# Optimization experiments

Hardware: AMD Instinct MI355X
Metric: run time of the kernel (lower is better)

The kernel has to match this reference:

```python
import jax, jax.numpy as jnp
import numpy as np

SIG = [1, 1, 1, 1, -1]  # Cl(4,1)
NVEC = 5
GA = 1 << NVEC  # 32


def _build_gp_table():
    # Cayley table for the geometric product on blades indexed by bitmask.
    G = np.zeros((GA, GA, GA), np.float32)
    for a in range(GA):
        for b in range(GA):
            s = 0
            t = a >> 1
            while t:
                s += bin(t & b).count('1')
                t >>= 1
            sign = -1.0 if (s & 1) else 1.0
            common = a & b
            for i in range(NVEC):
                if (common >> i) & 1:
                    sign *= SIG[i]
            G[a, b, a ^ b] = sign
    return G

GP_TABLE = jnp.asarray(_build_gp_table())


def geometric_product(x, y):
    return jnp.einsum('...i,...j,ijk->...k', x, y, GP_TABLE)


def manifold_norm(x):
    # normalize each multivector onto the unit sphere in R^32
    return x / (jnp.linalg.norm(x, axis=-1, keepdims=True) + 1e-6)


def versor_linear(x, W, b):
    # channel mixing shared across multivector components: x [..., in, ga]
    return jnp.einsum('...ig,oi->...og', x, W) + b


def layer_norm2d(x, w, b):
    # LayerNorm over last two dims [D, ga] jointly
    mu = jnp.mean(x, axis=(-2, -1), keepdims=True)
    var = jnp.var(x, axis=(-2, -1), keepdims=True)
    return (x - mu) / jnp.sqrt(var + 1e-5) * w + b


def attention(x, Wq, bq, Wk, bk, Wv, bv, Wo, bo, n_heads):
    B, S, D, G = x.shape
    dh = D // n_heads
    q = versor_linear(x, Wq, bq).reshape(B, S, n_heads, dh, G)
    k = versor_linear(x, Wk, bk).reshape(B, S, n_heads, dh, G)
    v = versor_linear(x, Wv, bv).reshape(B, S, n_heads, dh, G)
    scale = 1.0 / np.sqrt(dh * G).astype(np.float32)
    scores = jnp.einsum('bshdg,bthdg->bhst', q, k) * scale
    probs = jax.nn.softmax(scores, axis=-1)
    o = jnp.einsum('bhst,bthdg->bshdg', probs, v).reshape(B, S, D, G)
    return versor_linear(o, Wo, bo)


N_HEADS = 8


def forward(x, Wq, bq, Wk, bk, Wv, bv, Wo, bo, ln1_w, ln1_b, ln2_w, ln2_b,
            gamma1, gamma2, W1, b1, W2, b2, Wr, br, Wc, bc):
    L = Wq.shape[0]
    for l in range(L):
        h = attention(layer_norm2d(x, ln1_w[l], ln1_b[l]),
                      Wq[l], bq[l], Wk[l], bk[l], Wv[l], bv[l], Wo[l], bo[l], N_HEADS)
        x = manifold_norm(x + gamma1[l] * h)
        m = versor_linear(layer_norm2d(x, ln2_w[l], ln2_b[l]), W1[l], b1[l])
        m = versor_linear(jnp.tanh(m), W2[l], b2[l])
        x = manifold_norm(x + gamma2[l] * m)
    # RecursiveRotorAccumulator: log(S)-step inclusive scan of rotors
    delta = versor_linear(x, Wr, br)
    rot = 0.5 * delta
    rot = rot.at[..., 0].add(1.0)
    rot = manifold_norm(rot)
    S = x.shape[1]
    step = 1
    while step < S:
        left = rot[:, :-step]
        right = rot[:, step:]
        comb = manifold_norm(geometric_product(right, left))
        rot = jnp.concatenate([rot[:, :step], comb], axis=1)
        step *= 2
    pooled = rot[:, -1]  # [B, D, ga]
    logits = pooled.reshape(pooled.shape[0], -1) @ Wc.T + bc
    return logits


def setup_inputs() -> dict:
    key = jax.random.key(0)
    B, S, D, G, L, NC = 8, 256, 64, GA, 4, 1000
    E = 4 * D  # expansion hidden
    ks = jax.random.split(key, 16)
    sd = 0.02
    inp = {
        'x': jax.random.normal(ks[0], (B, S, D, G), jnp.float32),
        'Wq': jax.random.normal(ks[1], (L, D, D), jnp.float32) * sd,
        'bq': jnp.zeros((L, D, G), jnp.float32),
        'Wk': jax.random.normal(ks[2], (L, D, D), jnp.float32) * sd,
        'bk': jnp.zeros((L, D, G), jnp.float32),
        'Wv': jax.random.normal(ks[3], (L, D, D), jnp.float32) * sd,
        'bv': jnp.zeros((L, D, G), jnp.float32),
        'Wo': jax.random.normal(ks[4], (L, D, D), jnp.float32) * sd,
        'bo': jnp.zeros((L, D, G), jnp.float32),
        'ln1_w': jnp.ones((L, D, G), jnp.float32),
        'ln1_b': jnp.zeros((L, D, G), jnp.float32),
        'ln2_w': jnp.ones((L, D, G), jnp.float32),
        'ln2_b': jnp.zeros((L, D, G), jnp.float32),
        'gamma1': 1e-5 * jnp.ones((L, D, G), jnp.float32),
        'gamma2': 1e-5 * jnp.ones((L, D, G), jnp.float32),
        'W1': jax.random.normal(ks[5], (L, E, D), jnp.float32) * sd,
        'b1': jnp.zeros((L, E, G), jnp.float32),
        'W2': jax.random.normal(ks[6], (L, D, E), jnp.float32) * sd,
        'b2': jnp.zeros((L, D, G), jnp.float32),
        'Wr': jax.random.normal(ks[7], (D, D), jnp.float32) * sd,
        'br': jnp.zeros((D, G), jnp.float32),
        'Wc': jax.random.normal(ks[8], (NC, D * G), jnp.float32) * sd,
        'bc': jnp.zeros((NC,), jnp.float32),
    }
    return inp


def reference(x, Wq, bq, Wk, bk, Wv, bv, Wo, bo, ln1_w, ln1_b, ln2_w, ln2_b,
              gamma1, gamma2, W1, b1, W2, b2, Wr, br, Wc, bc):
    return forward(x, Wq, bq, Wk, bk, Wv, bv, Wo, bo, ln1_w, ln1_b, ln2_w, ln2_b,
                   gamma1, gamma2, W1, b1, W2, b2, Wr, br, Wc, bc)
```

## Files before the change

### kernel.cpp

```cpp
#include <hip/hip_runtime.h>
#include <hip/hip_bf16.h>

constexpr int kB  = 8;
constexpr int kS  = 256;
constexpr int kD  = 64;
constexpr int kG  = 32;
constexpr int kE  = 256;
constexpr int kNH = 8;
constexpr int kHD = 256;
constexpr int kDG = kD * kG;
constexpr int kT  = kB * kS;
constexpr int kNC = 1000;

using bf16x8 = __attribute__((ext_vector_type(8))) short;
using f32x4  = __attribute__((ext_vector_type(4))) float;

__device__ __forceinline__ short f2bf(float f) {
    unsigned u = __float_as_uint(f);
    unsigned r = (u + 0x7FFFu + ((u >> 16) & 1u)) >> 16;
    return (short)r;
}

__device__ __forceinline__ float tanh_fast(float x) {
    float a = fabsf(x);
    float e = __expf(-2.f * a);
    float t = (1.f - e) / (1.f + e);
    return copysignf(t, x);
}

__global__ __launch_bounds__(256) void cvtw_kernel(
    const float* __restrict__ Wq, const float* __restrict__ Wk,
    const float* __restrict__ Wv, const float* __restrict__ Wo,
    const float* __restrict__ W1, const float* __restrict__ W2,
    unsigned short* __restrict__ dst) {
    int idx = (blockIdx.x * 256 + threadIdx.x) * 4;
    const float* src; int off;
    if      (idx <  16384) { src = Wq; off = 0; }
    else if (idx <  32768) { src = Wk; off = 16384; }
    else if (idx <  49152) { src = Wv; off = 32768; }
    else if (idx <  65536) { src = Wo; off = 49152; }
    else if (idx < 131072) { src = W1; off = 65536; }
    else                   { src = W2; off = 131072; }
    const float4 v = *(const float4*)(src + (idx - off));
    *(short4*)&dst[idx] = make_short4(f2bf(v.x), f2bf(v.y), f2bf(v.z), f2bf(v.w));
}

__global__ __launch_bounds__(256) void ln_kernel(const float* __restrict__ Xin,
                                                 const float* __restrict__ w,
                                                 const float* __restrict__ b,
                                                 float* __restrict__ A) {
    int t = blockIdx.x, tid = threadIdx.x;
    const float* xp = Xin + (size_t)t * kDG;
    __shared__ float r1[256], r2[256];
    float v[8], s = 0.f, ss = 0.f;
#pragma unroll
    for (int j = 0; j < 8; j++) {
        float x = xp[tid + j * 256];
        v[j] = x; s += x; ss += x * x;
    }
    r1[tid] = s; r2[tid] = ss; __syncthreads();
    for (int o = 128; o > 0; o >>= 1) {
        if (tid < o) { r1[tid] += r1[tid + o]; r2[tid] += r2[tid + o]; }
        __syncthreads();
    }
    float mean = r1[0] * (1.f / kDG);
    float var  = r2[0] * (1.f / kDG) - mean * mean;
    float rstd = rsqrtf(var + 1e-5f);
    float* ao = A + (size_t)t * kDG;
#pragma unroll
    for (int j = 0; j < 8; j++) {
        int jj = tid + j * 256;
        ao[jj] = (v[j] - mean) * rstd * w[jj] + b[jj];
    }
}

__device__ __forceinline__ void epi_res_mn_ln(
    const f32x4 (&acc)[4][2], const float* __restrict__ bias,
    const float* __restrict__ Xin, float* __restrict__ Xout,
    const float* __restrict__ gamma,
    const float* __restrict__ lnw, const float* __restrict__ lnb,
    float* __restrict__ Aout, int tok, int l16, int quad, bool do_ln) {
    const size_t tb = (size_t)tok * kDG;
    float xv[4][2][4];
    float s = 0.f, ss = 0.f;
#pragma unroll
    for (int mt = 0; mt < 4; ++mt)
#pragma unroll
        for (int r = 0; r < 4; ++r) {
            int o = mt * 16 + quad * 4 + r;
            float vv[2]; float sq = 0.f;
#pragma unroll
            for (int nt = 0; nt < 2; ++nt) {
                int g = nt * 16 + l16;
                float h = acc[mt][nt][r] + bias[o * kG + g];
                float v = Xin[tb + o * kG + g] + gamma[o * kG + g] * h;
                vv[nt] = v; sq = fmaf(v, v, sq);
            }
#pragma unroll
            for (int off = 1; off < 16; off <<= 1) sq += __shfl_xor(sq, off, 64);
            float rn = 1.f / (sqrtf(sq) + 1e-6f);
#pragma unroll
            for (int nt = 0; nt < 2; ++nt) {
                int g = nt * 16 + l16;
                float x = vv[nt] * rn;
                xv[mt][nt][r] = x;
                Xout[tb + o * kG + g] = x;
                s += x; ss = fmaf(x, x, ss);
            }
        }
    if (!do_ln) return;
#pragma unroll
    for (int off = 1; off < 64; off <<= 1) {
        s += __shfl_xor(s, off, 64); ss += __shfl_xor(ss, off, 64);
    }
    float mean = s * (1.f / kDG);
    float var  = ss * (1.f / kDG) - mean * mean;
    float rstd = rsqrtf(var + 1e-5f);
#pragma unroll
    for (int mt = 0; mt < 4; ++mt)
#pragma unroll
        for (int nt = 0; nt < 2; ++nt) {
            int g = nt * 16 + l16;
#pragma unroll
            for (int r = 0; r < 4; ++r) {
                int o = mt * 16 + quad * 4 + r;
                Aout[tb + o * kG + g] = (xv[mt][nt][r] - mean) * rstd * lnw[o * kG + g] + lnb[o * kG + g];
            }
        }
}

__global__ __launch_bounds__(256) void vlinT_kernel(const float* __restrict__ X,
                                                    const float* __restrict__ W,
                                                    const float* __restrict__ bias,
                                                    float* __restrict__ OutT) {
    __shared__ float sx[kDG];
    __shared__ float sw[kD * kD];
    int t = blockIdx.x, tid = threadIdx.x;
    const float* xp = X + (size_t)t * kDG;
    for (int j = tid; j < kDG; j += 256) sx[j] = xp[j];
    for (int j = tid; j < kD * kD; j += 256) sw[j] = W[j];
    __syncthreads();
    int g = tid & 31, ob = tid >> 5;
    int b = t >> 8, s = t & 255;
    float* op = OutT + ((size_t)b * kD * kS + s) * kG;
    for (int o = ob; o < kD; o += 8) {
        float acc = bias[o * kG + g];
        const float* wr = sw + o * kD;
#pragma unroll
        for (int i = 0; i < kD; i++) acc += wr[i] * sx[i * kG + g];
        op[(size_t)o * kS * kG + g] = acc;
    }
}

__global__ __launch_bounds__(256, 2) void mlp1_kernel(
    const float* __restrict__ X, const unsigned short* __restrict__ Wh,
    const float* __restrict__ bias, unsigned short* __restrict__ outH) {
    constexpr int M = 256;
    constexpr int WS = 64 + 8;
    __shared__ short sW[M * WS];
    __shared__ short sXT[4][32][WS];

    const int tid = threadIdx.x, wave = tid >> 6, lane = tid & 63;
    const int l16 = lane & 15, quad = lane >> 4;
    const int tok = blockIdx.x * 4 + wave;

    for (int j = tid * 8; j < M * 64; j += 2048) {
        int o = j >> 6, i = j & 63;
        *(bf16x8*)&sW[o * WS + i] = *(const bf16x8*)(Wh + j);
    }
    {
        const int g4 = (lane & 7) * 4;
        const int i0 = (lane >> 3) * 8;
        const float* xp = X + (size_t)tok * kDG;
#pragma unroll
        for (int half = 0; half < 2; ++half) {
            float4 vr[4];
#pragma unroll
            for (int r = 0; r < 4; ++r)
                vr[r] = *(const float4*)(xp + (i0 + half * 4 + r) * kG + g4);
#pragma unroll
            for (int gg = 0; gg < 4; ++gg)
                *(short4*)&sXT[wave][g4 + gg][i0 + half * 4] =
                    make_short4(f2bf((&vr[0].x)[gg]), f2bf((&vr[1].x)[gg]),
                                f2bf((&vr[2].x)[gg]), f2bf((&vr[3].x)[gg]));
        }
    }
    __syncthreads();

    bf16x8 bfr[2][2];
#pragma unroll
    for (int c = 0; c < 2; ++c)
#pragma unroll
        for (int nt = 0; nt < 2; ++nt)
            bfr[c][nt] = *(const bf16x8*)&sXT[wave][nt * 16 + l16][c * 32 + quad * 8];

    f32x4 acc[16][2];
#pragma unroll
    for (int mt = 0; mt < 16; ++mt)
#pragma unroll
        for (int nt = 0; nt < 2; ++nt) acc[mt][nt] = (f32x4){0.f, 0.f, 0.f, 0.f};

#pragma unroll
    for (int mt = 0; mt < 16; ++mt)
#pragma unroll
        for (int c = 0; c < 2; ++c) {
            bf16x8 afr = *(const bf16x8*)&sW[(mt * 16 + l16) * WS + c * 32 + quad * 8];
#pragma unroll
            for (int nt = 0; nt < 2; ++nt)
                acc[mt][nt] = __builtin_amdgcn_mfma_f32_16x16x32_bf16(afr, bfr[c][nt], acc[mt][nt], 0, 0, 0);
        }

    unsigned short* op = outH + (size_t)tok * M * kG;
#pragma unroll
    for (int mt = 0; mt < 16; ++mt)
#pragma unroll
        for (int nt = 0; nt < 2; ++nt) {
            int g = nt * 16 + l16;
            int e0 = mt * 16 + quad * 4;
            short4 s4;
            s4.x = f2bf(tanh_fast(acc[mt][nt][0] + bias[(e0 + 0) * kG + g]));
            s4.y = f2bf(tanh_fast(acc[mt][nt][1] + bias[(e0 + 1) * kG + g]));
            s4.z = f2bf(tanh_fast(acc[mt][nt][2] + bias[(e0 + 2) * kG + g]));
            s4.w = f2bf(tanh_fast(acc[mt][nt][3] + bias[(e0 + 3) * kG + g]));
            *(short4*)&op[g * M + e0] = s4;
        }
}

__global__ __launch_bounds__(256, 2) void gemmWo_fused_kernel(
    const float* __restrict__ X, const unsigned short* __restrict__ Wh,
    const float* __restrict__ bias,
    const float* __restrict__ Xin, const float* __restrict__ gamma,
    const float* __restrict__ lnw, const float* __restrict__ lnb,
    float* __restrict__ Xout, float* __restrict__ Aout) {
    constexpr int WS = 64 + 8;
    __shared__ short sW[64 * WS];
    __shared__ short sXT[4][32][WS];

    const int tid = threadIdx.x, wave = tid >> 6, lane = tid & 63;
    const int l16 = lane & 15, quad = lane >> 4;
    const int tok = blockIdx.x * 4 + wave;

    for (int j = tid * 8; j < 64 * 64; j += 2048) {
        int o = j >> 6, i = j & 63;
        *(bf16x8*)&sW[o * WS + i] = *(const bf16x8*)(Wh + j);
    }
    {
        const int g4 = (lane & 7) * 4;
        const int i0 = (lane >> 3) * 8;
        const float* xp = X + (size_t)tok * kDG;
#pragma unroll
        for (int half = 0; half < 2; ++half) {
            float4 vr[4];
#pragma unroll
            for (int r = 0; r < 4; ++r)
                vr[r] = *(const float4*)(xp + (i0 + half * 4 + r) * kG + g4);
#pragma unroll
            for (int gg = 0; gg < 4; ++gg)
                *(short4*)&sXT[wave][g4 + gg][i0 + half * 4] =
                    make_short4(f2bf((&vr[0].x)[gg]), f2bf((&vr[1].x)[gg]),
                                f2bf((&vr[2].x)[gg]), f2bf((&vr[3].x)[gg]));
        }
    }
    __syncthreads();

    bf16x8 bfr[2][2];
#pragma unroll
    for (int c = 0; c < 2; ++c)
#pragma unroll
        for (int nt = 0; nt < 2; ++nt)
            bfr[c][nt] = *(const bf16x8*)&sXT[wave][nt * 16 + l16][c * 32 + quad * 8];

    f32x4 acc[4][2];
#pragma unroll
    for (int mt = 0; mt < 4; ++mt)
#pragma unroll
        for (int nt = 0; nt < 2; ++nt) acc[mt][nt] = (f32x4){0.f, 0.f, 0.f, 0.f};

#pragma unroll
    for (int mt = 0; mt < 4; ++mt)
#pragma unroll
        for (int c = 0; c < 2; ++c) {
            bf16x8 afr = *(const bf16x8*)&sW[(mt * 16 + l16) * WS + c * 32 + quad * 8];
#pragma unroll
            for (int nt = 0; nt < 2; ++nt)
                acc[mt][nt] = __builtin_amdgcn_mfma_f32_16x16x32_bf16(afr, bfr[c][nt], acc[mt][nt], 0, 0, 0);
        }

    epi_res_mn_ln(acc, bias, Xin, Xout, gamma, lnw, lnb, Aout, tok, l16, quad, true);
}

__global__ __launch_bounds__(256, 2) void gemm_qkv_kernel(
    const float* __restrict__ X,
    const unsigned short* __restrict__ Wqh, const unsigned short* __restrict__ Wkh,
    const unsigned short* __restrict__ Wvh,
    const float* __restrict__ bq, const float* __restrict__ bk, const float* __restrict__ bv,
    unsigned short* __restrict__ Q, unsigned short* __restrict__ K, unsigned short* __restrict__ V) {
    constexpr int WS = 64 + 8;
    __shared__ short sW[3 * 64 * WS];
    __shared__ short sXT[4][32][WS];

    const int tid = threadIdx.x, wave = tid >> 6, lane = tid & 63;
    const int l16 = lane & 15, quad = lane >> 4;
    const int tok = blockIdx.x * 4 + wave;

    const unsigned short* Wp[3] = {Wqh, Wkh, Wvh};
#pragma unroll
    for (int w = 0; w < 3; ++w)
        for (int j = tid * 8; j < 64 * 64; j += 2048) {
            int o = j >> 6, i = j & 63;
            *(bf16x8*)&sW[w * 64 * WS + o * WS + i] = *(const bf16x8*)(Wp[w] + j);
        }
    {
        const int g4 = (lane & 7) * 4;
        const int i0 = (lane >> 3) * 8;
        const float* xp = X + (size_t)tok * kDG;
#pragma unroll
        for (int half = 0; half < 2; ++half) {
            float4 vr[4];
#pragma unroll
            for (int r = 0; r < 4; ++r)
                vr[r] = *(const float4*)(xp + (i0 + half * 4 + r) * kG + g4);
#pragma unroll
            for (int gg = 0; gg < 4; ++gg)
                *(short4*)&sXT[wave][g4 + gg][i0 + half * 4] =
                    make_short4(f2bf((&vr[0].x)[gg]), f2bf((&vr[1].x)[gg]),
                                f2bf((&vr[2].x)[gg]), f2bf((&vr[3].x)[gg]));
        }
    }
    __syncthreads();

    bf16x8 bfr[2][2];
#pragma unroll
    for (int c = 0; c < 2; ++c)
#pragma unroll
        for (int nt = 0; nt < 2; ++nt)
            bfr[c][nt] = *(const bf16x8*)&sXT[wave][nt * 16 + l16][c * 32 + quad * 8];

    f32x4 acc[3][4][2];
#pragma unroll
    for (int w = 0; w < 3; ++w)
#pragma unroll
        for (int mt = 0; mt < 4; ++mt)
#pragma unroll
            for (int nt = 0; nt < 2; ++nt) acc[w][mt][nt] = (f32x4){0.f, 0.f, 0.f, 0.f};

#pragma unroll
    for (int w = 0; w < 3; ++w)
#pragma unroll
        for (int mt = 0; mt < 4; ++mt)
#pragma unroll
            for (int c = 0; c < 2; ++c) {
                bf16x8 afr = *(const bf16x8*)&sW[w * 64 * WS + (mt * 16 + l16) * WS + c * 32 + quad * 8];
#pragma unroll
                for (int nt = 0; nt < 2; ++nt)
                    acc[w][mt][nt] = __builtin_amdgcn_mfma_f32_16x16x32_bf16(afr, bfr[c][nt], acc[w][mt][nt], 0, 0, 0);
            }

    unsigned short* Op[3] = {Q, K, V};
    const float* Bp[3] = {bq, bk, bv};
#pragma unroll
    for (int w = 0; w < 3; ++w) {
        unsigned short* op = Op[w] + (size_t)tok * kDG;
#pragma unroll
        for (int mt = 0; mt < 4; ++mt)
#pragma unroll
            for (int nt = 0; nt < 2; ++nt) {
                int g = nt * 16 + l16;
#pragma unroll
                for (int r = 0; r < 4; ++r) {
                    int o = mt * 16 + quad * 4 + r;
                    op[o * kG + g] = (unsigned short)f2bf(acc[w][mt][nt][r] + Bp[w][o * kG + g]);
                }
            }
    }
}

template<bool DO_LN>
__global__ __launch_bounds__(256, 2) void mlp2_fused_kernel(
    const unsigned short* __restrict__ Mb,
    const unsigned short* __restrict__ W2h, const float* __restrict__ b2,
    float* __restrict__ X, const float* __restrict__ gamma,
    const float* __restrict__ lnw, const float* __restrict__ lnb,
    float* __restrict__ Aout) {
    constexpr int WS = 256 + 8;
    __shared__ short sW[64 * WS];
    const int tid = threadIdx.x, wave = tid >> 6, lane = tid & 63;
    const int l16 = lane & 15, quad = lane >> 4;
    const int tok = blockIdx.x * 4 + wave;

    for (int j = tid * 8; j < 64 * 256; j += 2048) {
        int o = j >> 8, i = j & 255;
        *(bf16x8*)&sW[o * WS + i] = *(const bf16x8*)(W2h + j);
    }
    __syncthreads();

    f32x4 acc[4][2];
#pragma unroll
    for (int mt = 0; mt < 4; ++mt)
#pragma unroll
        for (int nt = 0; nt < 2; ++nt) acc[mt][nt] = (f32x4){0.f, 0.f, 0.f, 0.f};

    const unsigned short* mp = Mb + (size_t)tok * kG * kE;
#pragma unroll
    for (int c = 0; c < 8; ++c) {
        bf16x8 bfr[2];
#pragma unroll
        for (int nt = 0; nt < 2; ++nt)
            bfr[nt] = *(const bf16x8*)&mp[(nt * 16 + l16) * kE + c * 32 + quad * 8];
#pragma unroll
        for (int mt = 0; mt < 4; ++mt) {
            bf16x8 afr = *(const bf16x8*)&sW[(mt * 16 + l16) * WS + c * 32 + quad * 8];
#pragma unroll
            for (int nt = 0; nt < 2; ++nt)
                acc[mt][nt] = __builtin_amdgcn_mfma_f32_16x16x32_bf16(afr, bfr[nt], acc[mt][nt], 0, 0, 0);
        }
    }

    epi_res_mn_ln(acc, b2, X, X, gamma, lnw, lnb, Aout, tok, l16, quad, DO_LN);
}

constexpr int QSTR = 264;
constexpr int VSTR = 40;

__global__ __launch_bounds__(256) void attn_mfma_kernel(const unsigned short* __restrict__ Q,
                                                        const unsigned short* __restrict__ K,
                                                        const unsigned short* __restrict__ V,
                                                        float* __restrict__ O) {
    __shared__ short sQ[64 * QSTR];
    __shared__ short sKV[256 * VSTR];

    const int qt = blockIdx.x, h = blockIdx.y, b = blockIdx.z;
    const int tid = threadIdx.x;
    const int wave = tid >> 6, lane = tid & 63;
    const int l16 = lane & 15, quad = lane >> 4;

    const size_t bh = (size_t)b * kS * kDG + (size_t)h * kHD;

#pragma unroll
    for (int it = 0; it < 8; ++it) {
        int j = it * 2048 + tid * 8;
        int row = j >> 8, col = j & 255;
        *(bf16x8*)&sQ[row * QSTR + col] =
            *(const bf16x8*)(Q + bh + (size_t)(qt * 64 + row) * kDG + col);
    }
    bf16x8 kpre[4];
#pragma unroll
    for (int it = 0; it < 4; ++it) {
        int j = it * 2048 + tid * 8;
        int row = j >> 8, col = j & 255;
        kpre[it] = *(const bf16x8*)(K + bh + (size_t)row * kDG + col);
    }
    __syncthreads();

    bf16x8 afrag[8];
    {
        int row = wave * 16 + l16;
#pragma unroll
        for (int c = 0; c < 8; ++c)
            afrag[c] = *(const bf16x8*)&sQ[row * QSTR + c * 32 + quad * 8];
    }

    f32x4 acc[16];
#pragma unroll
    for (int i = 0; i < 16; ++i) acc[i] = (f32x4){0.f, 0.f, 0.f, 0.f};

    for (int kt = 0; kt < 8; ++kt) {
#pragma unroll
        for (int it = 0; it < 4; ++it) {
            int j = it * 2048 + tid * 8;
            int row = j >> 8, col = j & 255;
            *(bf16x8*)&sKV[row * QSTR + col] = kpre[it];
        }
        __syncthreads();
        if (kt < 7) {
#pragma unroll
            for (int it = 0; it < 4; ++it) {
                int j = it * 2048 + tid * 8;
                int row = j >> 8, col = j & 255;
                kpre[it] = *(const bf16x8*)(K + bh + (size_t)((kt + 1) * 32 + row) * kDG + col);
            }
        }
#pragma unroll
        for (int nt = 0; nt < 2; ++nt) {
            int key = nt * 16 + l16;
            f32x4 a = acc[kt * 2 + nt];
#pragma unroll
            for (int c = 0; c < 8; ++c) {
                bf16x8 bfrag = *(const bf16x8*)&sKV[key * QSTR + c * 32 + quad * 8];
                a = __builtin_amdgcn_mfma_f32_16x16x32_bf16(afrag[c], bfrag, a, 0, 0, 0);
            }
            acc[kt * 2 + nt] = a;
        }
        __syncthreads();
    }

    float inv[4];
#pragma unroll
    for (int r = 0; r < 4; ++r) {
        float m = -1e30f;
#pragma unroll
        for (int t = 0; t < 16; ++t) m = fmaxf(m, acc[t][r]);
#pragma unroll
        for (int off = 1; off < 16; off <<= 1) m = fmaxf(m, __shfl_xor(m, off, 16));
        float s = 0.f;
#pragma unroll
        for (int t = 0; t < 16; ++t) {
            float p = __expf((acc[t][r] - m) * 0.0625f);
            acc[t][r] = p; s += p;
        }
#pragma unroll
        for (int off = 1; off < 16; off <<= 1) s += __shfl_xor(s, off, 16);
        inv[r] = 1.f / s;
    }

#pragma unroll
    for (int t = 0; t < 16; ++t)
#pragma unroll
        for (int r = 0; r < 4; ++r)
            sQ[(wave * 16 + quad * 4 + r) * QSTR + t * 16 + l16] = f2bf(acc[t][r]);

    short4 vpre[8];
    {
        int kb = tid >> 5;
#pragma unroll
        for (int it = 0; it < 2; ++it) {
            int db = (tid & 31) + it * 32;
#pragma unroll
            for (int r = 0; r < 4; ++r)
                vpre[it * 4 + r] = *(const short4*)(V + bh + (size_t)(kb * 4 + r) * kDG + db * 4);
        }
    }

    f32x4 oacc[16];
#pragma unroll
    for (int i = 0; i < 16; ++i) oacc[i] = (f32x4){0.f, 0.f, 0.f, 0.f};

    for (int vt = 0; vt < 8; ++vt) {
        __syncthreads();
        {
            int kb = tid >> 5;
#pragma unroll
            for (int it = 0; it < 2; ++it) {
                int db = (tid & 31) + it * 32;
#pragma unroll
                for (int i = 0; i < 4; ++i) {
                    short4 p = make_short4((&vpre[it * 4 + 0].x)[i], (&vpre[it * 4 + 1].x)[i],
                                           (&vpre[it * 4 + 2].x)[i], (&vpre[it * 4 + 3].x)[i]);
                    *(short4*)&sKV[(db * 4 + i) * VSTR + kb * 4] = p;
                }
            }
        }
        __syncthreads();
        if (vt < 7) {
            int kb = tid >> 5;
#pragma unroll
            for (int it = 0; it < 2; ++it) {
                int db = (tid & 31) + it * 32;
#pragma unroll
                for (int r = 0; r < 4; ++r)
                    vpre[it * 4 + r] = *(const short4*)(V + bh + (size_t)((vt + 1) * 32 + kb * 4 + r) * kDG + db * 4);
            }
        }
        bf16x8 pfrag = *(const bf16x8*)&sQ[(wave * 16 + l16) * QSTR + vt * 32 + quad * 8];
#pragma unroll
        for (int dt = 0; dt < 16; ++dt) {
            bf16x8 vfrag = *(const bf16x8*)&sKV[(dt * 16 + l16) * VSTR + quad * 8];
            oacc[dt] = __builtin_amdgcn_mfma_f32_16x16x32_bf16(pfrag, vfrag, oacc[dt], 0, 0, 0);
        }
    }

    {
        int qrow = qt * 64 + wave * 16 + quad * 4;
#pragma unroll
        for (int dt = 0; dt < 16; ++dt)
#pragma unroll
            for (int r = 0; r < 4; ++r)
                O[bh + (size_t)(qrow + r) * kDG + dt * 16 + l16] = oacc[dt][r] * inv[r];
    }
}

constexpr int pc_ce(unsigned v) { int c = 0; while (v) { c += v & 1; v >>= 1; } return c; }
constexpr unsigned gp_mask_ce(int a) {
    unsigned m = 0;
    for (int c = 0; c < 32; ++c) {
        int b = a ^ c;
        int s = (a & b) >> 4;
        for (int t = a >> 1; t; t >>= 1) s += pc_ce(t & b);
        if (s & 1) m |= (1u << c);
    }
    return m;
}

template<int A>
__device__ __forceinline__ void gp_term(const float* x, const float* y, float* acc) {
    constexpr unsigned m = gp_mask_ce(A);
    const float xa = x[A], nxa = -xa;
#pragma unroll
    for (int c = 0; c < 32; ++c)
        acc[c] = fmaf(((m >> c) & 1u) ? nxa : xa, y[A ^ c], acc[c]);
}

__device__ __forceinline__ void gp_mn_t(const float* x, const float* y, float* out) {
    float acc[32];
#pragma unroll
    for (int c = 0; c < 32; ++c) acc[c] = 0.f;
    gp_term<0>(x, y, acc);  gp_term<1>(x, y, acc);  gp_term<2>(x, y, acc);  gp_term<3>(x, y, acc);
    gp_term<4>(x, y, acc);  gp_term<5>(x, y, acc);  gp_term<6>(x, y, acc);  gp_term<7>(x, y, acc);
    gp_term<8>(x, y, acc);  gp_term<9>(x, y, acc);  gp_term<10>(x, y, acc); gp_term<11>(x, y, acc);
    gp_term<12>(x, y, acc); gp_term<13>(x, y, acc); gp_term<14>(x, y, acc); gp_term<15>(x, y, acc);
    gp_term<16>(x, y, acc); gp_term<17>(x, y, acc); gp_term<18>(x, y, acc); gp_term<19>(x, y, acc);
    gp_term<20>(x, y, acc); gp_term<21>(x, y, acc); gp_term<22>(x, y, acc); gp_term<23>(x, y, acc);
    gp_term<24>(x, y, acc); gp_term<25>(x, y, acc); gp_term<26>(x, y, acc); gp_term<27>(x, y, acc);
    gp_term<28>(x, y, acc); gp_term<29>(x, y, acc); gp_term<30>(x, y, acc); gp_term<31>(x, y, acc);
    float ss = 0.f;
#pragma unroll
    for (int c = 0; c < 32; ++c) ss = fmaf(acc[c], acc[c], ss);
    float r = 1.f / (sqrtf(ss) + 1e-6f);
#pragma unroll
    for (int c = 0; c < 32; ++c) out[c] = acc[c] * r;
}

__device__ __forceinline__ void leaf_load(const float* base, float* v) {
#pragma unroll
    for (int i = 0; i < 8; ++i) {
        const float4 f = *(const float4*)(base + i * 4);
        v[i * 4 + 0] = 0.5f * f.x; v[i * 4 + 1] = 0.5f * f.y;
        v[i * 4 + 2] = 0.5f * f.z; v[i * 4 + 3] = 0.5f * f.w;
    }
    v[0] += 1.f;
    float ss = 0.f;
#pragma unroll
    for (int c = 0; c < 32; ++c) ss = fmaf(v[c], v[c], ss);
    float r = 1.f / (sqrtf(ss) + 1e-6f);
#pragma unroll
    for (int c = 0; c < 32; ++c) v[c] *= r;
}

__global__ __launch_bounds__(256) void scanreg_kernel(const float* __restrict__ DT,
                                                      float* __restrict__ pooled) {
    const int wave = threadIdx.x >> 6, lane = threadIdx.x & 63;
    const int seq = blockIdx.x * 4 + wave;
    const float* base = DT + ((size_t)seq * kS + lane * 4) * kG;

    float R[32], Y[32], P[32], Xa[32], Yb[32];

    leaf_load(base, R);
    for (int j = 1; j < 4; ++j) {
        leaf_load(base + j * kG, Y);
        gp_mn_t(Y, R, R);
    }

    for (int step = 1; step < 64; step <<= 1) {
        const bool up = lane & step;
#pragma unroll
        for (int c = 0; c < 32; ++c) P[c] = __shfl_xor(R[c], step, 64);
#pragma unroll
        for (int c = 0; c < 32; ++c) {
            Xa[c] = up ? R[c] : P[c];
            Yb[c] = up ? P[c] : R[c];
        }
        gp_mn_t(Xa, Yb, R);
    }

    if (lane == 0) {
        float* op = pooled + (size_t)seq * kG;
#pragma unroll
        for (int i = 0; i < 8; ++i)
            *(float4*)(op + i * 4) = make_float4(R[i * 4], R[i * 4 + 1], R[i * 4 + 2], R[i * 4 + 3]);
    }
}

__global__ __launch_bounds__(256) void cls2_kernel(const float* __restrict__ P,
                                                   const float* __restrict__ Wc,
                                                   const float* __restrict__ bc,
                                                   float* __restrict__ out) {
    __shared__ float sp[kB * kDG];
    const int tid = threadIdx.x, wave = tid >> 6, lane = tid & 63;
    for (int j = tid * 4; j < kB * kDG; j += 1024)
        *(float4*)&sp[j] = *(const float4*)(P + j);
    __syncthreads();

    const int c = blockIdx.x * 4 + wave;
    const float* w = Wc + (size_t)c * kDG;
    float acc[kB];
#pragma unroll
    for (int b = 0; b < kB; ++b) acc[b] = 0.f;
#pragma unroll
    for (int cc = 0; cc < 8; ++cc) {
        const float4 w4 = *(const float4*)(w + cc * 256 + lane * 4);
#pragma unroll
        for (int b = 0; b < kB; ++b) {
            const float4 p4 = *(const float4*)&sp[b * kDG + cc * 256 + lane * 4];
            acc[b] += w4.x * p4.x + w4.y * p4.y + w4.z * p4.z + w4.w * p4.w;
        }
    }
#pragma unroll
    for (int b = 0; b < kB; ++b)
#pragma unroll
        for (int off = 32; off > 0; off >>= 1) acc[b] += __shfl_xor(acc[b], off, 64);
    if (lane == 0) {
        float bias = bc[c];
#pragma unroll
        for (int b = 0; b < kB; ++b) out[b * kNC + c] = acc[b] + bias;
    }
}

extern "C" void kernel_launch(void* const* d_in, const int* in_sizes, int n_in,
                              void* d_out, int out_size, void* d_ws, size_t ws_size,
                              hipStream_t stream) {
    const float* x_in = (const float*)d_in[0];
    const float* Wq   = (const float*)d_in[1];
    const float* bq   = (const float*)d_in[2];
    const float* Wk   = (const float*)d_in[3];
    const float* bk   = (const float*)d_in[4];
    const float* Wv   = (const float*)d_in[5];
    const float* bv   = (const float*)d_in[6];
    const float* Wo   = (const float*)d_in[7];
    const float* bo   = (const float*)d_in[8];
    const float* ln1w = (const float*)d_in[9];
    const float* ln1b = (const float*)d_in[10];
    const float* ln2w = (const float*)d_in[11];
    const float* ln2b = (const float*)d_in[12];
    const float* gm1  = (const float*)d_in[13];
    const float* gm2  = (const float*)d_in[14];
    const float* W1   = (const float*)d_in[15];
    const float* b1   = (const float*)d_in[16];
    const float* W2   = (const float*)d_in[17];
    const float* b2   = (const float*)d_in[18];
    const float* Wr   = (const float*)d_in[19];
    const float* br   = (const float*)d_in[20];
    const float* Wc   = (const float*)d_in[21];
    const float* bc   = (const float*)d_in[22];

    const size_t NEL = (size_t)kT * kDG;
    float* F  = (float*)d_ws;
    float* X  = F;
    float* A  = F + NEL;
    unsigned short* Qh = (unsigned short*)(F + 2 * NEL);
    unsigned short* Kh = (unsigned short*)(F + 3 * NEL);
    unsigned short* Vh = (unsigned short*)(F + 4 * NEL);
    unsigned short* Mb = (unsigned short*)(F + 3 * NEL);
    unsigned short* Wb = (unsigned short*)(F + 5 * NEL);
    float* pooled = F + 2 * NEL;
    float* DT = A;

    cvtw_kernel<<<192, 256, 0, stream>>>(Wq, Wk, Wv, Wo, W1, W2, Wb);
    unsigned short* Wqh = Wb;
    unsigned short* Wkh = Wb + 16384;
    unsigned short* Wvh = Wb + 32768;
    unsigned short* Woh = Wb + 49152;
    unsigned short* W1h = Wb + 65536;
    unsigned short* W2h = Wb + 131072;

    ln_kernel<<<kT, 256, 0, stream>>>(x_in, ln1w, ln1b, A);

    for (int l = 0; l < 4; l++) {
        gemm_qkv_kernel<<<kT / 4, 256, 0, stream>>>(A,
            Wqh + l * 4096, Wkh + l * 4096, Wvh + l * 4096,
            bq + l * kDG, bk + l * kDG, bv + l * kDG, Qh, Kh, Vh);
        attn_mfma_kernel<<<dim3(4, kNH, kB), 256, 0, stream>>>(Qh, Kh, Vh, A);
        gemmWo_fused_kernel<<<kT / 4, 256, 0, stream>>>(A, Woh + l * 4096, bo + l * kDG,
            l == 0 ? x_in : X, gm1 + l * kDG, ln2w + l * kDG, ln2b + l * kDG, X, A);
        mlp1_kernel<<<kT / 4, 256, 0, stream>>>(A, W1h + l * 16384, b1 + l * kE * kG, Mb);
        if (l < 3)
            mlp2_fused_kernel<true><<<kT / 4, 256, 0, stream>>>(Mb, W2h + l * 16384, b2 + l * kDG,
                X, gm2 + l * kDG, ln1w + (l + 1) * kDG, ln1b + (l + 1) * kDG, A);
        else
            mlp2_fused_kernel<false><<<kT / 4, 256, 0, stream>>>(Mb, W2h + l * 16384, b2 + l * kDG,
                X, gm2 + l * kDG, nullptr, nullptr, nullptr);
    }

    vlinT_kernel<<<kT, 256, 0, stream>>>(X, Wr, br, DT);
    scanreg_kernel<<<kB * kD / 4, 256, 0, stream>>>(DT, pooled);
    cls2_kernel<<<kNC / 4, 256, 0, stream>>>(pooled, Wc, bc, (float*)d_out);
}
```

Measured before the change: 560.6 us.

## Double-buffer K/V shared tiles in attention and raise GEMM occupancy bounds

The attention kernel now uses two shared-memory K/V buffers. The next tile is written into the alternate buffer after the current tile's MFMAs, which cuts the block-wide barriers per K and V iteration from two to one and lets the global loads overlap with compute. Separately, the QKV, Wo and MLP2 GEMM kernels raise their minimum blocks per SM in launch_bounds from 2 to 3. This tightens the register budget to allow more resident blocks, at the risk of register spills. The attention kernel's shared-memory footprint also grows by one K/V buffer, which may lower its occupancy.

```diff
diff --git a/kernel.cpp b/kernel.cpp
--- a/kernel.cpp
+++ b/kernel.cpp
@@ -226,7 +226,7 @@
         }
 }
 
-__global__ __launch_bounds__(256, 2) void gemmWo_fused_kernel(
+__global__ __launch_bounds__(256, 3) void gemmWo_fused_kernel(
     const float* __restrict__ X, const unsigned short* __restrict__ Wh,
     const float* __restrict__ bias,
     const float* __restrict__ Xin, const float* __restrict__ gamma,
@@ -289,7 +289,7 @@
     epi_res_mn_ln(acc, bias, Xin, Xout, gamma, lnw, lnb, Aout, tok, l16, quad, true);
 }
 
-__global__ __launch_bounds__(256, 2) void gemm_qkv_kernel(
+__global__ __launch_bounds__(256, 3) void gemm_qkv_kernel(
     const float* __restrict__ X,
     const unsigned short* __restrict__ Wqh, const unsigned short* __restrict__ Wkh,
     const unsigned short* __restrict__ Wvh,
@@ -376,7 +376,7 @@
 }
 
 template<bool DO_LN>
-__global__ __launch_bounds__(256, 2) void mlp2_fused_kernel(
+__global__ __launch_bounds__(256, 3) void mlp2_fused_kernel(
     const unsigned short* __restrict__ Mb,
     const unsigned short* __restrict__ W2h, const float* __restrict__ b2,
     float* __restrict__ X, const float* __restrict__ gamma,
@@ -427,7 +427,7 @@
                                                         const unsigned short* __restrict__ V,
                                                         float* __restrict__ O) {
     __shared__ short sQ[64 * QSTR];
-    __shared__ short sKV[256 * VSTR];
+    __shared__ short sKV[2][256 * VSTR];
 
     const int qt = blockIdx.x, h = blockIdx.y, b = blockIdx.z;
     const int tid = threadIdx.x;
@@ -443,12 +443,12 @@
         *(bf16x8*)&sQ[row * QSTR + col] =
             *(const bf16x8*)(Q + bh + (size_t)(qt * 64 + row) * kDG + col);
     }
-    bf16x8 kpre[4];
 #pragma unroll
     for (int it = 0; it < 4; ++it) {
         int j = it * 2048 + tid * 8;
         int row = j >> 8, col = j & 255;
-        kpre[it] = *(const bf16x8*)(K + bh + (size_t)row * kDG + col);
+        *(bf16x8*)&sKV[0][row * QSTR + col] =
+            *(const bf16x8*)(K + bh + (size_t)row * kDG + col);
     }
     __syncthreads();
 
@@ -465,13 +465,7 @@
     for (int i = 0; i < 16; ++i) acc[i] = (f32x4){0.f, 0.f, 0.f, 0.f};
 
     for (int kt = 0; kt < 8; ++kt) {
-#pragma unroll
-        for (int it = 0; it < 4; ++it) {
-            int j = it * 2048 + tid * 8;
-            int row = j >> 8, col = j & 255;
-            *(bf16x8*)&sKV[row * QSTR + col] = kpre[it];
-        }
-        __syncthreads();
+        bf16x8 kpre[4];
         if (kt < 7) {
 #pragma unroll
             for (int it = 0; it < 4; ++it) {
@@ -480,18 +474,28 @@
                 kpre[it] = *(const bf16x8*)(K + bh + (size_t)((kt + 1) * 32 + row) * kDG + col);
             }
         }
+        const short* kb = sKV[kt & 1];
 #pragma unroll
         for (int nt = 0; nt < 2; ++nt) {
             int key = nt * 16 + l16;
             f32x4 a = acc[kt * 2 + nt];
 #pragma unroll
             for (int c = 0; c < 8; ++c) {
-                bf16x8 bfrag = *(const bf16x8*)&sKV[key * QSTR + c * 32 + quad * 8];
+                bf16x8 bfrag = *(const bf16x8*)&kb[key * QSTR + c * 32 + quad * 8];
                 a = __builtin_amdgcn_mfma_f32_16x16x32_bf16(afrag[c], bfrag, a, 0, 0, 0);
             }
             acc[kt * 2 + nt] = a;
         }
-        __syncthreads();
+        if (kt < 7) {
+            short* nb = sKV[(kt + 1) & 1];
+#pragma unroll
+            for (int it = 0; it < 4; ++it) {
+                int j = it * 2048 + tid * 8;
+                int row = j >> 8, col = j & 255;
+                *(bf16x8*)&nb[row * QSTR + col] = kpre[it];
+            }
+            __syncthreads();
+        }
     }
 
     float inv[4];
@@ -519,25 +523,50 @@
         for (int r = 0; r < 4; ++r)
             sQ[(wave * 16 + quad * 4 + r) * QSTR + t * 16 + l16] = f2bf(acc[t][r]);
 
-    short4 vpre[8];
     {
         int kb = tid >> 5;
 #pragma unroll
         for (int it = 0; it < 2; ++it) {
             int db = (tid & 31) + it * 32;
+            short4 vr[4];
 #pragma unroll
             for (int r = 0; r < 4; ++r)
-                vpre[it * 4 + r] = *(const short4*)(V + bh + (size_t)(kb * 4 + r) * kDG + db * 4);
-        }
-    }
+                vr[r] = *(const short4*)(V + bh + (size_t)(kb * 4 + r) * kDG + db * 4);
+#pragma unroll
+            for (int i = 0; i < 4; ++i) {
+                short4 p = make_short4((&vr[0].x)[i], (&vr[1].x)[i],
+                                       (&vr[2].x)[i], (&vr[3].x)[i]);
+                *(short4*)&sKV[0][(db * 4 + i) * VSTR + kb * 4] = p;
+            }
+        }
+    }
+    __syncthreads();
 
     f32x4 oacc[16];
 #pragma unroll
     for (int i = 0; i < 16; ++i) oacc[i] = (f32x4){0.f, 0.f, 0.f, 0.f};
 
     for (int vt = 0; vt < 8; ++vt) {
-        __syncthreads();
-        {
+        short4 vpre[8];
+        if (vt < 7) {
+            int kb = tid >> 5;
+#pragma unroll
+            for (int it = 0; it < 2; ++it) {
+                int db = (tid & 31) + it * 32;
+#pragma unroll
+                for (int r = 0; r < 4; ++r)
+                    vpre[it * 4 + r] = *(const short4*)(V + bh + (size_t)((vt + 1) * 32 + kb * 4 + r) * kDG + db * 4);
+            }
+        }
+        const short* vb = sKV[vt & 1];
+        bf16x8 pfrag = *(const bf16x8*)&sQ[(wave * 16 + l16) * QSTR + vt * 32 + quad * 8];
+#pragma unroll
+        for (int dt = 0; dt < 16; ++dt) {
+            bf16x8 vfrag = *(const bf16x8*)&vb[(dt * 16 + l16) * VSTR + quad * 8];
+            oacc[dt] = __builtin_amdgcn_mfma_f32_16x16x32_bf16(pfrag, vfrag, oacc[dt], 0, 0, 0);
+        }
+        if (vt < 7) {
+            short* nb = sKV[(vt + 1) & 1];
             int kb = tid >> 5;
 #pragma unroll
             for (int it = 0; it < 2; ++it) {
@@ -546,26 +575,10 @@
                 for (int i = 0; i < 4; ++i) {
                     short4 p = make_short4((&vpre[it * 4 + 0].x)[i], (&vpre[it * 4 + 1].x)[i],
                                            (&vpre[it * 4 + 2].x)[i], (&vpre[it * 4 + 3].x)[i]);
-                    *(short4*)&sKV[(db * 4 + i) * VSTR + kb * 4] = p;
+                    *(short4*)&nb[(db * 4 + i) * VSTR + kb * 4] = p;
                 }
             }
-        }
-        __syncthreads();
-        if (vt < 7) {
-            int kb = tid >> 5;
-#pragma unroll
-            for (int it = 0; it < 2; ++it) {
-                int db = (tid & 31) + it * 32;
-#pragma unroll
-                for (int r = 0; r < 4; ++r)
-                    vpre[it * 4 + r] = *(const short4*)(V + bh + (size_t)((vt + 1) * 32 + kb * 4 + r) * kDG + db * 4);
-            }
-        }
-        bf16x8 pfrag = *(const bf16x8*)&sQ[(wave * 16 + l16) * QSTR + vt * 32 + quad * 8];
-#pragma unroll
-        for (int dt = 0; dt < 16; ++dt) {
-            bf16x8 vfrag = *(const bf16x8*)&sKV[(dt * 16 + l16) * VSTR + quad * 8];
-            oacc[dt] = __builtin_amdgcn_mfma_f32_16x16x32_bf16(pfrag, vfrag, oacc[dt], 0, 0, 0);
+            __syncthreads();
         }
     }
 
```

Result: faster. 539.3 us (-3.8%).
